# Optimization experiments

Measured on AMD Instinct MI355X. Metric: run time of the kernel, lower is better.

Reference implementation:

```python
import jax, jax.numpy as jnp
import numpy as np

DIM = 2048
N_HEADS = 16
HEAD_DIM = DIM // N_HEADS
HIDDEN = 8192
BSZ = 2
SEQ = 2048
EPS = 1e-6


def setup_inputs() -> dict:
    key = jax.random.key(0)
    ks = jax.random.split(key, 8)
    x = jax.random.normal(ks[0], (BSZ, SEQ, DIM), dtype=jnp.float32)
    # causal additive mask, broadcastable to [B, H, S, S]
    mask = jnp.where(jnp.tril(jnp.ones((SEQ, SEQ), dtype=bool)), 0.0, -1e9)
    mask = mask[None, None, :, :].astype(jnp.float32)
    s = 0.02
    # torch.nn.Linear weights have shape [out_features, in_features]
    wq = jax.random.normal(ks[1], (DIM, DIM), dtype=jnp.float32) * s
    wk = jax.random.normal(ks[2], (DIM, DIM), dtype=jnp.float32) * s
    wv = jax.random.normal(ks[3], (DIM, DIM), dtype=jnp.float32) * s
    wo = jax.random.normal(ks[4], (DIM, DIM), dtype=jnp.float32) * s
    w1 = jax.random.normal(ks[5], (HIDDEN, DIM), dtype=jnp.float32) * s
    w2 = jax.random.normal(ks[6], (DIM, HIDDEN), dtype=jnp.float32) * s
    attn_norm_w = jnp.ones((DIM,), dtype=jnp.float32)
    ffn_norm_w = jnp.ones((DIM,), dtype=jnp.float32)
    return {"x": x, "mask": mask, "wq": wq, "wk": wk, "wv": wv, "wo": wo,
            "w1": w1, "w2": w2, "attn_norm_w": attn_norm_w, "ffn_norm_w": ffn_norm_w}


def rmsnorm(x, w):
    return x * jax.lax.rsqrt(jnp.mean(x * x, axis=-1, keepdims=True) + EPS) * w


def attention(x, mask, wq, wk, wv, wo):
    b, s, _ = x.shape
    q = (x @ wq.T).reshape(b, s, N_HEADS, HEAD_DIM)
    k = (x @ wk.T).reshape(b, s, N_HEADS, HEAD_DIM)
    v = (x @ wv.T).reshape(b, s, N_HEADS, HEAD_DIM)
    scores = jnp.einsum('bqhd,bkhd->bhqk', q, k) / jnp.sqrt(jnp.float32(HEAD_DIM))
    scores = scores + mask
    probs = jax.nn.softmax(scores, axis=-1)
    out = jnp.einsum('bhqk,bkhd->bqhd', probs, v).reshape(b, s, DIM)
    return out @ wo.T


def reference(x, mask, wq, wk, wv, wo, w1, w2, attn_norm_w, ffn_norm_w):
    h = x + attention(rmsnorm(x, attn_norm_w), mask, wq, wk, wv, wo)
    ffn_in = rmsnorm(h, ffn_norm_w)
    ffn = jax.nn.relu(ffn_in @ w1.T) @ w2.T
    return h + ffn
```

## Files before the change

### kernel.cpp

```cpp
#include <hip/hip_runtime.h>
#include <cstdint>
#include <cstddef>

#define DIM 2048
#define NHEADS 16
#define HD 128
#define HIDDEN 8192
#define BSZ 2
#define SEQ 2048
#define MTOT (BSZ*SEQ)

typedef __bf16 bf16_t;
typedef __bf16 bf16x8 __attribute__((ext_vector_type(8)));
typedef __bf16 bf16x4 __attribute__((ext_vector_type(4)));
typedef float  f32x4  __attribute__((ext_vector_type(4)));

__device__ __forceinline__ void gload16(const void* g, void* lds) {
  __builtin_amdgcn_global_load_lds(
      (const __attribute__((address_space(1))) uint32_t*)g,
      (__attribute__((address_space(3))) uint32_t*)lds, 16, 0, 0);
}

#define BAR() do { __builtin_amdgcn_sched_barrier(0); \
  asm volatile("s_barrier" ::: "memory"); \
  __builtin_amdgcn_sched_barrier(0); } while (0)
#define VMW(N) asm volatile("s_waitcnt vmcnt(" #N ")" ::: "memory")

__global__ void cvt_k(const float* __restrict__ src, bf16_t* __restrict__ dst, int n4) {
  int i = blockIdx.x * blockDim.x + threadIdx.x;
  int stride = gridDim.x * blockDim.x;
  for (; i < n4; i += stride) {
    float4 v = ((const float4*)src)[i];
    bf16x4 o = {(__bf16)v.x, (__bf16)v.y, (__bf16)v.z, (__bf16)v.w};
    ((bf16x4*)dst)[i] = o;
  }
}

__global__ __launch_bounds__(256)
void rmsnorm_k(const float* __restrict__ x, const float* __restrict__ wt,
               bf16_t* __restrict__ out) {
  const int row = blockIdx.x;
  const float* xr = x + (size_t)row * DIM;
  const int tid = threadIdx.x;
  float4 a = ((const float4*)xr)[tid];
  float4 b = ((const float4*)xr)[tid + 256];
  float ss = a.x*a.x + a.y*a.y + a.z*a.z + a.w*a.w
           + b.x*b.x + b.y*b.y + b.z*b.z + b.w*b.w;
  #pragma unroll
  for (int d = 32; d >= 1; d >>= 1) ss += __shfl_xor(ss, d, 64);
  __shared__ float red[4];
  if ((tid & 63) == 0) red[tid >> 6] = ss;
  __syncthreads();
  float tot = red[0] + red[1] + red[2] + red[3];
  float rs = rsqrtf(tot * (1.0f / DIM) + 1e-6f);
  float4 wa = ((const float4*)wt)[tid];
  float4 wb = ((const float4*)wt)[tid + 256];
  bf16x4 oa = {(__bf16)(a.x*rs*wa.x), (__bf16)(a.y*rs*wa.y),
               (__bf16)(a.z*rs*wa.z), (__bf16)(a.w*rs*wa.w)};
  bf16x4 ob = {(__bf16)(b.x*rs*wb.x), (__bf16)(b.y*rs*wb.y),
               (__bf16)(b.z*rs*wb.z), (__bf16)(b.w*rs*wb.w)};
  *(bf16x4*)(out + (size_t)row*DIM + tid*4)        = oa;
  *(bf16x4*)(out + (size_t)row*DIM + 1024 + tid*4) = ob;
}

template<int MH, int NH>
__device__ __forceinline__ void mm16(f32x4 (&acc)[8][4],
                                     const bf16x8 (&aF)[4][2],
                                     const bf16x8 (&bF)[2][2]) {
  __builtin_amdgcn_s_setprio(1);
  #pragma unroll
  for (int mt = 0; mt < 4; ++mt)
    #pragma unroll
    for (int nt = 0; nt < 2; ++nt)
      #pragma unroll
      for (int kk = 0; kk < 2; ++kk)
        acc[MH*4+mt][NH*2+nt] = __builtin_amdgcn_mfma_f32_16x16x32_bf16(
            aF[mt][kk], bF[nt][kk], acc[MH*4+mt][NH*2+nt], 0, 0, 0);
  __builtin_amdgcn_s_setprio(0);
}

__device__ __forceinline__ void rdA4(bf16x8 (&aF)[4][2], const bf16_t* rbase,
                                     int wr, int l16, int g) {
  #pragma unroll
  for (int mt = 0; mt < 4; ++mt)
    #pragma unroll
    for (int kk = 0; kk < 2; ++kk)
      aF[mt][kk] = *(const bf16x8*)((const char*)rbase +
          (wr*64 + mt*16 + l16)*128 + ((((kk<<2) ^ g) ^ (l16 & 7)) << 4));
}
__device__ __forceinline__ void rdB2(bf16x8 (&bF)[2][2], const bf16_t* rbase,
                                     int wc, int l16, int g) {
  #pragma unroll
  for (int nt = 0; nt < 2; ++nt)
    #pragma unroll
    for (int kk = 0; kk < 2; ++kk)
      bF[nt][kk] = *(const bf16x8*)((const char*)rbase +
          (wc*32 + nt*16 + l16)*128 + ((((kk<<2) ^ g) ^ (l16 & 7)) << 4));
}

template<typename OUT_T, bool RELU, bool HAS_RES, bool VT_OUT>
__global__ __launch_bounds__(512, 2)
void gemm8p(const bf16_t* __restrict__ A, const bf16_t* __restrict__ B,
            OUT_T* __restrict__ C, const float* __restrict__ res,
            int M, int N, int K) {
  __shared__ bf16_t sA[2][2][128*64];
  __shared__ bf16_t sB[2][2][128*64];
  const int tid  = threadIdx.x;
  const int lane = tid & 63;
  const int wid  = tid >> 6;
  const int l16  = lane & 15;
  const int g    = lane >> 4;
  const int wr   = wid >> 2;
  const int wc   = wid & 3;

  const int nwg = gridDim.x, bid = blockIdx.x;
  const int qq = nwg >> 3, rr = nwg & 7;
  const int xcd = bid & 7, loc = bid >> 3;
  const int wg = (xcd < rr ? xcd*(qq+1) : rr*(qq+1) + (xcd-rr)*qq) + loc;
  const int nbn = N >> 8;
  const int bm = (wg / nbn) << 8;
  const int bn = (wg % nbn) << 8;

  const int lr  = tid >> 3;
  const int cq8 = (((tid & 7) ^ (lr & 7)) << 3);

  const size_t aR = (size_t)(bm + lr) * K + cq8;
  const size_t bR = (size_t)(bn + ((lr >> 5) << 6) + (lr & 31)) * K + cq8;
  const size_t rowK128 = (size_t)128 * K, rowK64 = (size_t)64 * K, rowK32 = (size_t)32 * K;

  auto stA = [&](int buf, int mh, int kt) {
    const size_t ko = aR + (size_t)kt * 64 + (size_t)mh * rowK64;
    gload16(A + ko,            &sA[buf][mh][wid*512]);
    gload16(A + ko + rowK128,  &sA[buf][mh][4096 + wid*512]);
  };
  auto stB = [&](int buf, int nh, int kt) {
    const size_t ko = bR + (size_t)kt * 64 + (size_t)nh * rowK32;
    gload16(B + ko,              &sB[buf][nh][wid*512]);
    gload16(B + ko + 2*rowK64,   &sB[buf][nh][4096 + wid*512]);
  };

  f32x4 acc[8][4] = {};
  bf16x8 aF[4][2], bLo[2][2], bHi[2][2];

  stA(0, 0, 0); stB(0, 0, 0); stB(0, 1, 0); stA(0, 1, 0);
  stA(1, 0, 1); stB(1, 0, 1); stB(1, 1, 1);
  VMW(6);
  BAR();

  const int ni = K >> 7;
  for (int j = 0; j < ni; ++j) {
    const int t1 = 2*j + 1, t2 = 2*j + 2, t3 = 2*j + 3;
    const bool more = (j + 1 < ni);
    rdA4(aF, &sA[0][0][0], wr, l16, g);
    rdB2(bLo, &sB[0][0][0], wc, l16, g);
    stA(1, 1, t1);
    BAR();
    mm16<0,0>(acc, aF, bLo);
    BAR();
    rdB2(bHi, &sB[0][1][0], wc, l16, g);
    if (more) stA(0, 0, t2);
    BAR();
    mm16<0,1>(acc, aF, bHi);
    BAR();
    rdA4(aF, &sA[0][1][0], wr, l16, g);
    if (more) stB(0, 0, t2);
    BAR();
    mm16<1,1>(acc, aF, bHi);
    BAR();
    if (more) { stB(0, 1, t2); VMW(6); } else { VMW(0); }
    BAR();
    mm16<1,0>(acc, aF, bLo);
    BAR();
    rdA4(aF, &sA[1][0][0], wr, l16, g);
    rdB2(bLo, &sB[1][0][0], wc, l16, g);
    if (more) stA(0, 1, t2);
    BAR();
    mm16<0,0>(acc, aF, bLo);
    BAR();
    rdB2(bHi, &sB[1][1][0], wc, l16, g);
    if (more) stA(1, 0, t3);
    BAR();
    mm16<0,1>(acc, aF, bHi);
    BAR();
    rdA4(aF, &sA[1][1][0], wr, l16, g);
    if (more) stB(1, 0, t3);
    BAR();
    mm16<1,1>(acc, aF, bHi);
    BAR();
    if (more) { stB(1, 1, t3); VMW(6); }
    BAR();
    mm16<1,0>(acc, aF, bLo);
    BAR();
  }

  if (VT_OUT) {
    #pragma unroll
    for (int am = 0; am < 8; ++am) {
      const int row = bm + wr*128 + am*16 + g*4;
      #pragma unroll
      for (int an = 0; an < 4; ++an) {
        const int col = bn + wc*64 + an*16 + l16;
        f32x4 a4 = acc[am][an];
        bf16x4 v4 = {(__bf16)a4[0], (__bf16)a4[1], (__bf16)a4[2], (__bf16)a4[3]};
        *(bf16x4*)((bf16_t*)C +
            (((size_t)(row >> 11) * NHEADS + (col >> 7)) * HD + (col & 127)) * SEQ
            + (row & 2047)) = v4;
      }
    }
  } else {
    #pragma unroll
    for (int am = 0; am < 8; ++am) {
      #pragma unroll
      for (int r = 0; r < 4; ++r) {
        const int row = bm + wr*128 + am*16 + g*4 + r;
        #pragma unroll
        for (int an = 0; an < 4; ++an) {
          const int col = bn + wc*64 + an*16 + l16;
          float v = acc[am][an][r];
          if (HAS_RES) v += res[(size_t)row * N + col];
          if (RELU)    v = fmaxf(v, 0.0f);
          C[(size_t)row * N + col] = (OUT_T)v;
        }
      }
    }
  }
}

template<int MH, int NH>
__device__ __forceinline__ void mm8(f32x4 (&acc)[4][4],
                                    const bf16x8 (&aF)[2][2],
                                    const bf16x8 (&bF)[2][2]) {
  __builtin_amdgcn_s_setprio(1);
  #pragma unroll
  for (int mt = 0; mt < 2; ++mt)
    #pragma unroll
    for (int nt = 0; nt < 2; ++nt)
      #pragma unroll
      for (int kk = 0; kk < 2; ++kk)
        acc[MH*2+mt][NH*2+nt] = __builtin_amdgcn_mfma_f32_16x16x32_bf16(
            aF[mt][kk], bF[nt][kk], acc[MH*2+mt][NH*2+nt], 0, 0, 0);
  __builtin_amdgcn_s_setprio(0);
}

__device__ __forceinline__ void rd2(bf16x8 (&f)[2][2], const bf16_t* rbase,
                                    int wrow, int l16, int g) {
  #pragma unroll
  for (int t = 0; t < 2; ++t)
    #pragma unroll
    for (int kk = 0; kk < 2; ++kk)
      f[t][kk] = *(const bf16x8*)((const char*)rbase +
          (wrow + t*16 + l16)*128 + ((((kk<<2) ^ g) ^ (l16 & 7)) << 4));
}

template<typename OUT_T, bool RELU, bool HAS_RES, bool VT_OUT>
__global__ __launch_bounds__(512, 2)
void gemm8p_n128(const bf16_t* __restrict__ A, const bf16_t* __restrict__ B,
                 OUT_T* __restrict__ C, const float* __restrict__ res,
                 int M, int N, int K) {
  __shared__ bf16_t sA[2][2][128*64];
  __shared__ bf16_t sB[2][2][64*64];
  const int tid  = threadIdx.x;
  const int lane = tid & 63;
  const int wid  = tid >> 6;
  const int l16  = lane & 15;
  const int g    = lane >> 4;
  const int wr   = wid >> 1;
  const int wc   = wid & 1;

  const int nwg = gridDim.x, bid = blockIdx.x;
  const int qq = nwg >> 3, rr = nwg & 7;
  const int xcd = bid & 7, loc = bid >> 3;
  const int wg = (xcd < rr ? xcd*(qq+1) : rr*(qq+1) + (xcd-rr)*qq) + loc;
  const int nbn = N >> 7;
  const int bm = (wg / nbn) << 8;
  const int bn = (wg % nbn) << 7;

  const int lr  = tid >> 3;
  const int cq8 = (((tid & 7) ^ (lr & 7)) << 3);
  const size_t aR = (size_t)(bm + ((lr >> 5) << 6) + (lr & 31)) * K + cq8;
  const size_t bR = (size_t)(bn + ((lr >> 5) << 6) + (lr & 31)) * K + cq8;
  const size_t rowK128 = (size_t)128 * K, rowK32 = (size_t)32 * K;

  auto stA = [&](int buf, int mh, int kt) {
    const size_t ko = aR + (size_t)kt * 64 + (size_t)mh * rowK32;
    gload16(A + ko,            &sA[buf][mh][wid*512]);
    gload16(A + ko + rowK128,  &sA[buf][mh][4096 + wid*512]);
  };
  auto stB = [&](int buf, int nh, int kt) {
    gload16(B + bR + (size_t)kt * 64 + (size_t)nh * rowK32, &sB[buf][nh][wid*512]);
  };

  f32x4 acc[4][4] = {};
  bf16x8 aF[2][2], bLo[2][2], bHi[2][2];

  stA(0, 0, 0); stB(0, 0, 0); stB(0, 1, 0); stA(0, 1, 0);
  stA(1, 0, 1); stB(1, 0, 1); stB(1, 1, 1);
  VMW(4);
  BAR();

  const int ar = wr*32;
  const int br = wc*32;
  const int ni = K >> 7;
  for (int j = 0; j < ni; ++j) {
    const int t1 = 2*j + 1, t2 = 2*j + 2, t3 = 2*j + 3;
    const bool more = (j + 1 < ni);
    rd2(aF,  &sA[0][0][0], ar, l16, g);
    rd2(bLo, &sB[0][0][0], br, l16, g);
    stA(1, 1, t1);
    BAR();
    mm8<0,0>(acc, aF, bLo);
    BAR();
    rd2(bHi, &sB[0][1][0], br, l16, g);
    if (more) stA(0, 0, t2);
    BAR();
    mm8<0,1>(acc, aF, bHi);
    BAR();
    rd2(aF, &sA[0][1][0], ar, l16, g);
    if (more) stB(0, 0, t2);
    BAR();
    mm8<1,1>(acc, aF, bHi);
    BAR();
    if (more) { stB(0, 1, t2); VMW(4); } else { VMW(0); }
    BAR();
    mm8<1,0>(acc, aF, bLo);
    BAR();
    rd2(aF,  &sA[1][0][0], ar, l16, g);
    rd2(bLo, &sB[1][0][0], br, l16, g);
    if (more) stA(0, 1, t2);
    BAR();
    mm8<0,0>(acc, aF, bLo);
    BAR();
    rd2(bHi, &sB[1][1][0], br, l16, g);
    if (more) stA(1, 0, t3);
    BAR();
    mm8<0,1>(acc, aF, bHi);
    BAR();
    rd2(aF, &sA[1][1][0], ar, l16, g);
    if (more) stB(1, 0, t3);
    BAR();
    mm8<1,1>(acc, aF, bHi);
    BAR();
    if (more) { stB(1, 1, t3); VMW(4); }
    BAR();
    mm8<1,0>(acc, aF, bLo);
    BAR();
  }

  if (VT_OUT) {
    #pragma unroll
    for (int am = 0; am < 4; ++am) {
      const int row = bm + wr*64 + am*16 + g*4;
      #pragma unroll
      for (int an = 0; an < 4; ++an) {
        const int col = bn + wc*64 + an*16 + l16;
        f32x4 a4 = acc[am][an];
        bf16x4 v4 = {(__bf16)a4[0], (__bf16)a4[1], (__bf16)a4[2], (__bf16)a4[3]};
        *(bf16x4*)((bf16_t*)C +
            (((size_t)(row >> 11) * NHEADS + (col >> 7)) * HD + (col & 127)) * SEQ
            + (row & 2047)) = v4;
      }
    }
  } else {
    #pragma unroll
    for (int am = 0; am < 4; ++am) {
      #pragma unroll
      for (int r = 0; r < 4; ++r) {
        const int row = bm + wr*64 + am*16 + g*4 + r;
        #pragma unroll
        for (int an = 0; an < 4; ++an) {
          const int col = bn + wc*64 + an*16 + l16;
          float v = acc[am][an][r];
          if (HAS_RES) v += res[(size_t)row * N + col];
          if (RELU)    v = fmaxf(v, 0.0f);
          C[(size_t)row * N + col] = (OUT_T)v;
        }
      }
    }
  }
}

__global__ __launch_bounds__(256, 2)
void attn_k(const bf16_t* __restrict__ Q, const bf16_t* __restrict__ Kk,
            const bf16_t* __restrict__ VT, bf16_t* __restrict__ O) {
  __shared__ bf16_t sK[2][64 * 128];
  __shared__ bf16_t sVT[2][128 * 64];
  __shared__ bf16_t sP[4][32 * 64];
  const int tid = threadIdx.x, lane = tid & 63, w = tid >> 6;
  const int l16 = lane & 15, g = lane >> 4;
  const int b = blockIdx.z, h = blockIdx.y;
  const int qt = b ? (SEQ/128 - 1 - blockIdx.x) : blockIdx.x;
  const int ch = h * HD;
  const size_t gb = (size_t)b * SEQ * DIM;
  const int qbase = qt*128 + w*32;
  const bf16_t* VTh = VT + ((size_t)b * NHEADS + h) * ((size_t)HD * SEQ);

  bf16x8 qf[2][4];
  #pragma unroll
  for (int mt = 0; mt < 2; ++mt)
    #pragma unroll
    for (int kb = 0; kb < 4; ++kb)
      qf[mt][kb] = *(const bf16x8*)(Q + gb + (size_t)(qbase + mt*16 + l16)*DIM + ch + kb*32 + g*8);

  f32x4 o[2][8] = {};
  float m_r[2][4], l_r[2][4];
  #pragma unroll
  for (int mt = 0; mt < 2; ++mt)
    #pragma unroll
    for (int r = 0; r < 4; ++r) { m_r[mt][r] = -1e9f; l_r[mt][r] = 0.0f; }

  const float rs = 0.08838834764831845f;
  const int nsteps = (qt*128 + 128) >> 6;

  auto stageK = [&](int buf, int kv0) {
    #pragma unroll
    for (int i = 0; i < 4; ++i) {
      const int c = i*256 + tid;
      const int kv = c >> 4, pos = c & 15;
      const int qsrc = pos ^ (kv & 7);
      gload16(Kk + gb + (size_t)(kv0 + kv)*DIM + ch + (qsrc << 3),
              (char*)sK[buf] + (size_t)(i*256 + w*64)*16);
    }
  };
  auto stageVT = [&](int buf, int kv0) {
    #pragma unroll
    for (int i = 0; i < 4; ++i) {
      const int c = i*256 + tid;
      const int d = c >> 3, p = c & 7;
      const int q = p ^ (d & 7);
      gload16(VTh + (size_t)d * SEQ + kv0 + (q << 3),
              (char*)sVT[buf] + (size_t)(i*256 + w*64)*16);
    }
  };

  stageK(0, 0);  stageVT(0, 0);
  if (nsteps > 1) { stageK(1, 64); stageVT(1, 64); }
  __syncthreads();

  int cur = 0;
  for (int t = 0; t < nsteps; ++t) {
    const int kv0 = t << 6;
    const bool active = (kv0 < qbase + 32);
    if (active) {
      f32x4 s[2][4] = {};
      const char* kb_ = (const char*)sK[cur];
      #pragma unroll
      for (int nt = 0; nt < 4; ++nt) {
        const int row = nt*16 + l16;
        #pragma unroll
        for (int kbi = 0; kbi < 4; ++kbi) {
          const int pos = (kbi*4 + g) ^ (l16 & 7);
          bf16x8 kf = *(const bf16x8*)(kb_ + row*256 + (pos << 4));
          #pragma unroll
          for (int mt = 0; mt < 2; ++mt)
            s[mt][nt] = __builtin_amdgcn_mfma_f32_16x16x32_bf16(qf[mt][kbi], kf, s[mt][nt], 0, 0, 0);
        }
      }

      const bool needmask = (kv0 + 63 > qbase);
      char* pb = (char*)sP[w];
      #pragma unroll
      for (int mt = 0; mt < 2; ++mt) {
        #pragma unroll
        for (int r = 0; r < 4; ++r) {
          const int qpos = qbase + mt*16 + g*4 + r;
          float sv[4];
          #pragma unroll
          for (int nt = 0; nt < 4; ++nt) {
            sv[nt] = s[mt][nt][r] * rs;
            if (needmask && (kv0 + nt*16 + l16 > qpos)) sv[nt] = -1e9f;
          }
          float mx = fmaxf(fmaxf(sv[0], sv[1]), fmaxf(sv[2], sv[3]));
          #pragma unroll
          for (int d = 8; d >= 1; d >>= 1) mx = fmaxf(mx, __shfl_xor(mx, d, 16));
          const float mo = m_r[mt][r];
          if (mx > mo) {
            const float sc = __expf(mo - mx);
            l_r[mt][r] *= sc;
            #pragma unroll
            for (int dt = 0; dt < 8; ++dt) o[mt][dt][r] *= sc;
            m_r[mt][r] = mx;
          }
          const float mn = m_r[mt][r];
          float p[4], rsum = 0.0f;
          #pragma unroll
          for (int nt = 0; nt < 4; ++nt) { p[nt] = __expf(sv[nt] - mn); rsum += p[nt]; }
          #pragma unroll
          for (int d = 8; d >= 1; d >>= 1) rsum += __shfl_xor(rsum, d, 16);
          l_r[mt][r] += rsum;
          const int prow = mt*16 + g*4 + r;
          #pragma unroll
          for (int nt = 0; nt < 4; ++nt)
            *(bf16_t*)(pb + ((prow*128 + nt*32 + l16*2) ^ (g << 5))) = (bf16_t)p[nt];
        }
      }

      bf16x8 pa[2][2];
      #pragma unroll
      for (int mt = 0; mt < 2; ++mt) {
        const int row2 = mt*16 + l16;
        #pragma unroll
        for (int ks = 0; ks < 2; ++ks)
          pa[mt][ks] = *(const bf16x8*)((const char*)sP[w] +
                    ((row2*128 + ks*64 + g*16) ^ (((l16 >> 2) & 3) << 5)));
      }

      const char* vb_ = (const char*)sVT[cur];
      #pragma unroll
      for (int dt = 0; dt < 8; ++dt) {
        const int d = dt*16 + l16;
        #pragma unroll
        for (int ks = 0; ks < 2; ++ks) {
          const int pos = (ks*4 + g) ^ (d & 7);
          bf16x8 vf = *(const bf16x8*)(vb_ + d*128 + (pos << 4));
          #pragma unroll
          for (int mt = 0; mt < 2; ++mt)
            o[mt][dt] = __builtin_amdgcn_mfma_f32_16x16x32_bf16(pa[mt][ks], vf, o[mt][dt], 0, 0, 0);
        }
      }
    }
    __syncthreads();
    if (t + 2 < nsteps) {
      stageK(cur, (t + 2) << 6);
      stageVT(cur, (t + 2) << 6);
    }
    cur ^= 1;
  }

  #pragma unroll
  for (int mt = 0; mt < 2; ++mt) {
    #pragma unroll
    for (int r = 0; r < 4; ++r) {
      const float inv = 1.0f / l_r[mt][r];
      const int row = qbase + mt*16 + g*4 + r;
      #pragma unroll
      for (int dt = 0; dt < 8; ++dt)
        O[gb + (size_t)row*DIM + ch + dt*16 + l16] = (bf16_t)(o[mt][dt][r] * inv);
    }
  }
}

extern "C" void kernel_launch(void* const* d_in, const int* in_sizes, int n_in,
                              void* d_out, int out_size, void* d_ws, size_t ws_size,
                              hipStream_t stream) {
  const float* x   = (const float*)d_in[0];
  const float* wq  = (const float*)d_in[2];
  const float* wk  = (const float*)d_in[3];
  const float* wv  = (const float*)d_in[4];
  const float* wo  = (const float*)d_in[5];
  const float* w1  = (const float*)d_in[6];
  const float* w2  = (const float*)d_in[7];
  const float* anw = (const float*)d_in[8];
  const float* fnw = (const float*)d_in[9];
  float* out = (float*)d_out;

  char* p = (char*)d_ws;
  bf16_t* wqb = (bf16_t*)p; p += (size_t)DIM*DIM*2;
  bf16_t* wkb = (bf16_t*)p; p += (size_t)DIM*DIM*2;
  bf16_t* wvb = (bf16_t*)p; p += (size_t)DIM*DIM*2;
  bf16_t* wob = (bf16_t*)p; p += (size_t)DIM*DIM*2;
  bf16_t* w1b = (bf16_t*)p; p += (size_t)DIM*HIDDEN*2;
  bf16_t* w2b = (bf16_t*)p; p += (size_t)DIM*HIDDEN*2;
  bf16_t* xn  = (bf16_t*)p; p += (size_t)MTOT*DIM*2;
  float*  hb  = (float*)p;  p += (size_t)MTOT*DIM*4;
  bf16_t* big = (bf16_t*)p; p += (size_t)MTOT*HIDDEN*2;
  bf16_t* qb = big;
  bf16_t* kb = big + (size_t)MTOT*DIM;
  bf16_t* vT = big + 2*(size_t)MTOT*DIM;
  bf16_t* ab = big + 3*(size_t)MTOT*DIM;
  bf16_t* f1 = big;

  auto cvt = [&](const float* s, bf16_t* d, size_t n) {
    int n4 = (int)(n / 4);
    int blocks = (n4 + 255) / 256; if (blocks > 4096) blocks = 4096;
    cvt_k<<<blocks, 256, 0, stream>>>(s, d, n4);
  };
  cvt(wq, wqb, (size_t)DIM*DIM);
  cvt(wk, wkb, (size_t)DIM*DIM);
  cvt(wv, wvb, (size_t)DIM*DIM);
  cvt(wo, wob, (size_t)DIM*DIM);
  cvt(w1, w1b, (size_t)DIM*HIDDEN);
  cvt(w2, w2b, (size_t)DIM*HIDDEN);

  rmsnorm_k<<<MTOT, 256, 0, stream>>>(x, anw, xn);

  gemm8p_n128<bf16_t, false, false, false><<<256, 512, 0, stream>>>(xn, wqb, qb, nullptr, MTOT, DIM, DIM);
  gemm8p_n128<bf16_t, false, false, false><<<256, 512, 0, stream>>>(xn, wkb, kb, nullptr, MTOT, DIM, DIM);
  gemm8p_n128<bf16_t, false, false, true ><<<256, 512, 0, stream>>>(xn, wvb, vT, nullptr, MTOT, DIM, DIM);

  attn_k<<<dim3(SEQ/128, NHEADS, BSZ), 256, 0, stream>>>(qb, kb, vT, ab);

  gemm8p_n128<float, false, true, false><<<256, 512, 0, stream>>>(ab, wob, hb, x, MTOT, DIM, DIM);

  rmsnorm_k<<<MTOT, 256, 0, stream>>>(hb, fnw, xn);

  gemm8p<bf16_t, true, false, false><<<512, 512, 0, stream>>>(xn, w1b, f1, nullptr, MTOT, HIDDEN, DIM);

  gemm8p_n128<float, false, true, false><<<256, 512, 0, stream>>>(f1, w2b, out, hb, MTOT, DIM, HIDDEN);
}
```

Baseline: 657.1 us.

## Fuse QKV projection, batch weight casts, split-K FFN down-proj, exp2 softmax

Merges the six weight-conversion launches into one kernel and the three Q/K/V projections into a single GEMM over the concatenated weight, with an epilogue that routes each tile to q, k, or the transposed v buffer. The FFN down-projection switches to a split-K-by-2 run of the 256x256 GEMM that writes two fp32 partials, followed by a reduction kernel that adds the residual. In attention, the softmax scale and log2(e) are folded into Q once so the loop can use exp2f, and MFMA sections are bracketed with setprio. This cuts launch overhead and adds wave parallelism, at the cost of extra fp32 partial traffic, an extra reduction pass, and a bf16 rounding of the scaled Q.

Result: no change. 650.8 us (-1.0%).

```diff
diff --git a/kernel.cpp b/kernel.cpp
--- a/kernel.cpp
+++ b/kernel.cpp
@@ -26,11 +26,25 @@
   __builtin_amdgcn_sched_barrier(0); } while (0)
 #define VMW(N) asm volatile("s_waitcnt vmcnt(" #N ")" ::: "memory")
 
-__global__ void cvt_k(const float* __restrict__ src, bf16_t* __restrict__ dst, int n4) {
+__global__ void cvt_all_k(const float* __restrict__ wq, const float* __restrict__ wk,
+                          const float* __restrict__ wv, const float* __restrict__ wo,
+                          const float* __restrict__ w1, const float* __restrict__ w2,
+                          bf16_t* __restrict__ dst) {
+  const int S1 = (DIM*DIM) >> 2;
+  const int S2 = (DIM*HIDDEN) >> 2;
+  const int total = 4*S1 + 2*S2;
   int i = blockIdx.x * blockDim.x + threadIdx.x;
-  int stride = gridDim.x * blockDim.x;
-  for (; i < n4; i += stride) {
-    float4 v = ((const float4*)src)[i];
+  const int stride = gridDim.x * blockDim.x;
+  for (; i < total; i += stride) {
+    const float* src; int off;
+    if (i < 4*S1) {
+      const int r = i >> 20; off = i & (S1 - 1);
+      src = (r == 0) ? wq : (r == 1) ? wk : (r == 2) ? wv : wo;
+    } else {
+      const int j = i - 4*S1;
+      if (j < S2) { src = w1; off = j; } else { src = w2; off = j - S2; }
+    }
+    float4 v = ((const float4*)src)[off];
     bf16x4 o = {(__bf16)v.x, (__bf16)v.y, (__bf16)v.z, (__bf16)v.w};
     ((bf16x4*)dst)[i] = o;
   }
@@ -63,6 +77,19 @@
   *(bf16x4*)(out + (size_t)row*DIM + 1024 + tid*4) = ob;
 }
 
+__global__ void reduce2_k(const float* __restrict__ hb, const float* __restrict__ p1,
+                          float* __restrict__ out, int n4) {
+  int i = blockIdx.x * blockDim.x + threadIdx.x;
+  const int stride = gridDim.x * blockDim.x;
+  for (; i < n4; i += stride) {
+    float4 a = ((const float4*)out)[i];
+    float4 h = ((const float4*)hb)[i];
+    float4 b = ((const float4*)p1)[i];
+    float4 o = {h.x + a.x + b.x, h.y + a.y + b.y, h.z + a.z + b.z, h.w + a.w + b.w};
+    ((float4*)out)[i] = o;
+  }
+}
+
 template<int MH, int NH>
 __device__ __forceinline__ void mm16(f32x4 (&acc)[8][4],
                                      const bf16x8 (&aF)[4][2],
@@ -98,11 +125,11 @@
           (wc*32 + nt*16 + l16)*128 + ((((kk<<2) ^ g) ^ (l16 & 7)) << 4));
 }
 
-template<typename OUT_T, bool RELU, bool HAS_RES, bool VT_OUT>
+template<typename OUT_T, bool RELU, bool HAS_RES, int SPLIT>
 __global__ __launch_bounds__(512, 2)
 void gemm8p(const bf16_t* __restrict__ A, const bf16_t* __restrict__ B,
             OUT_T* __restrict__ C, const float* __restrict__ res,
-            int M, int N, int K) {
+            int M, int N, int K, int Klen) {
   __shared__ bf16_t sA[2][2][128*64];
   __shared__ bf16_t sB[2][2][128*64];
   const int tid  = threadIdx.x;
@@ -117,9 +144,18 @@
   const int qq = nwg >> 3, rr = nwg & 7;
   const int xcd = bid & 7, loc = bid >> 3;
   const int wg = (xcd < rr ? xcd*(qq+1) : rr*(qq+1) + (xcd-rr)*qq) + loc;
+
+  int tile = wg;
+  if (SPLIT > 1) {
+    const int slice = wg % SPLIT;
+    tile = wg / SPLIT;
+    A += (size_t)slice * Klen;
+    B += (size_t)slice * Klen;
+    if (slice) C = (OUT_T*)res;
+  }
   const int nbn = N >> 8;
-  const int bm = (wg / nbn) << 8;
-  const int bn = (wg % nbn) << 8;
+  const int bm = (tile / nbn) << 8;
+  const int bn = (tile % nbn) << 8;
 
   const int lr  = tid >> 3;
   const int cq8 = (((tid & 7) ^ (lr & 7)) << 3);
@@ -147,7 +183,7 @@
   VMW(6);
   BAR();
 
-  const int ni = K >> 7;
+  const int ni = Klen >> 7;
   for (int j = 0; j < ni; ++j) {
     const int t1 = 2*j + 1, t2 = 2*j + 2, t3 = 2*j + 3;
     const bool more = (j + 1 < ni);
@@ -193,34 +229,18 @@
     BAR();
   }
 
-  if (VT_OUT) {
-    #pragma unroll
-    for (int am = 0; am < 8; ++am) {
-      const int row = bm + wr*128 + am*16 + g*4;
+  #pragma unroll
+  for (int am = 0; am < 8; ++am) {
+    #pragma unroll
+    for (int r = 0; r < 4; ++r) {
+      const int row = bm + wr*128 + am*16 + g*4 + r;
       #pragma unroll
       for (int an = 0; an < 4; ++an) {
         const int col = bn + wc*64 + an*16 + l16;
-        f32x4 a4 = acc[am][an];
-        bf16x4 v4 = {(__bf16)a4[0], (__bf16)a4[1], (__bf16)a4[2], (__bf16)a4[3]};
-        *(bf16x4*)((bf16_t*)C +
-            (((size_t)(row >> 11) * NHEADS + (col >> 7)) * HD + (col & 127)) * SEQ
-            + (row & 2047)) = v4;
-      }
-    }
-  } else {
-    #pragma unroll
-    for (int am = 0; am < 8; ++am) {
-      #pragma unroll
-      for (int r = 0; r < 4; ++r) {
-        const int row = bm + wr*128 + am*16 + g*4 + r;
-        #pragma unroll
-        for (int an = 0; an < 4; ++an) {
-          const int col = bn + wc*64 + an*16 + l16;
-          float v = acc[am][an][r];
-          if (HAS_RES) v += res[(size_t)row * N + col];
-          if (RELU)    v = fmaxf(v, 0.0f);
-          C[(size_t)row * N + col] = (OUT_T)v;
-        }
+        float v = acc[am][an][r];
+        if (HAS_RES) v += res[(size_t)row * N + col];
+        if (RELU)    v = fmaxf(v, 0.0f);
+        C[(size_t)row * N + col] = (OUT_T)v;
       }
     }
   }
@@ -252,7 +272,7 @@
           (wrow + t*16 + l16)*128 + ((((kk<<2) ^ g) ^ (l16 & 7)) << 4));
 }
 
-template<typename OUT_T, bool RELU, bool HAS_RES, bool VT_OUT>
+template<typename OUT_T, bool RELU, bool HAS_RES, int OMODE>
 __global__ __launch_bounds__(512, 2)
 void gemm8p_n128(const bf16_t* __restrict__ A, const bf16_t* __restrict__ B,
                  OUT_T* __restrict__ C, const float* __restrict__ res,
@@ -346,18 +366,37 @@
     BAR();
   }
 
-  if (VT_OUT) {
-    #pragma unroll
-    for (int am = 0; am < 4; ++am) {
-      const int row = bm + wr*64 + am*16 + g*4;
-      #pragma unroll
-      for (int an = 0; an < 4; ++an) {
-        const int col = bn + wc*64 + an*16 + l16;
-        f32x4 a4 = acc[am][an];
-        bf16x4 v4 = {(__bf16)a4[0], (__bf16)a4[1], (__bf16)a4[2], (__bf16)a4[3]};
-        *(bf16x4*)((bf16_t*)C +
-            (((size_t)(row >> 11) * NHEADS + (col >> 7)) * HD + (col & 127)) * SEQ
-            + (row & 2047)) = v4;
+  if (OMODE == 2) {
+    const int t = bn >> 11;
+    const int clb = bn & 2047;
+    if (t < 2) {
+      bf16_t* base = (bf16_t*)C + (size_t)t * MTOT * DIM;
+      #pragma unroll
+      for (int am = 0; am < 4; ++am) {
+        #pragma unroll
+        for (int r = 0; r < 4; ++r) {
+          const int row = bm + wr*64 + am*16 + g*4 + r;
+          #pragma unroll
+          for (int an = 0; an < 4; ++an) {
+            const int cl = clb + wc*64 + an*16 + l16;
+            base[(size_t)row * DIM + cl] = (bf16_t)acc[am][an][r];
+          }
+        }
+      }
+    } else {
+      bf16_t* vbase = (bf16_t*)C + (size_t)2 * MTOT * DIM;
+      #pragma unroll
+      for (int am = 0; am < 4; ++am) {
+        const int row = bm + wr*64 + am*16 + g*4;
+        #pragma unroll
+        for (int an = 0; an < 4; ++an) {
+          const int cl = clb + wc*64 + an*16 + l16;
+          f32x4 a4 = acc[am][an];
+          bf16x4 v4 = {(__bf16)a4[0], (__bf16)a4[1], (__bf16)a4[2], (__bf16)a4[3]};
+          *(bf16x4*)(vbase +
+              (((size_t)(row >> 11) * NHEADS + (cl >> 7)) * HD + (cl & 127)) * SEQ
+              + (row & 2047)) = v4;
+        }
       }
     }
   } else {
@@ -401,6 +440,15 @@
     for (int kb = 0; kb < 4; ++kb)
       qf[mt][kb] = *(const bf16x8*)(Q + gb + (size_t)(qbase + mt*16 + l16)*DIM + ch + kb*32 + g*8);
 
+  const float qs = 0.08838834764831845f * 1.44269504088896f;
+  #pragma unroll
+  for (int mt = 0; mt < 2; ++mt)
+    #pragma unroll
+    for (int kb = 0; kb < 4; ++kb)
+      #pragma unroll
+      for (int e = 0; e < 8; ++e)
+        qf[mt][kb][e] = (__bf16)((float)qf[mt][kb][e] * qs);
+
   f32x4 o[2][8] = {};
   float m_r[2][4], l_r[2][4];
   #pragma unroll
@@ -408,7 +456,6 @@
     #pragma unroll
     for (int r = 0; r < 4; ++r) { m_r[mt][r] = -1e9f; l_r[mt][r] = 0.0f; }
 
-  const float rs = 0.08838834764831845f;
   const int nsteps = (qt*128 + 128) >> 6;
 
   auto stageK = [&](int buf, int kv0) {
@@ -443,6 +490,7 @@
     if (active) {
       f32x4 s[2][4] = {};
       const char* kb_ = (const char*)sK[cur];
+      __builtin_amdgcn_s_setprio(1);
       #pragma unroll
       for (int nt = 0; nt < 4; ++nt) {
         const int row = nt*16 + l16;
@@ -455,6 +503,7 @@
             s[mt][nt] = __builtin_amdgcn_mfma_f32_16x16x32_bf16(qf[mt][kbi], kf, s[mt][nt], 0, 0, 0);
         }
       }
+      __builtin_amdgcn_s_setprio(0);
 
       const bool needmask = (kv0 + 63 > qbase);
       char* pb = (char*)sP[w];
@@ -466,7 +515,7 @@
           float sv[4];
           #pragma unroll
           for (int nt = 0; nt < 4; ++nt) {
-            sv[nt] = s[mt][nt][r] * rs;
+            sv[nt] = s[mt][nt][r];
             if (needmask && (kv0 + nt*16 + l16 > qpos)) sv[nt] = -1e9f;
           }
           float mx = fmaxf(fmaxf(sv[0], sv[1]), fmaxf(sv[2], sv[3]));
@@ -474,7 +523,7 @@
           for (int d = 8; d >= 1; d >>= 1) mx = fmaxf(mx, __shfl_xor(mx, d, 16));
           const float mo = m_r[mt][r];
           if (mx > mo) {
-            const float sc = __expf(mo - mx);
+            const float sc = exp2f(mo - mx);
             l_r[mt][r] *= sc;
             #pragma unroll
             for (int dt = 0; dt < 8; ++dt) o[mt][dt][r] *= sc;
@@ -483,7 +532,7 @@
           const float mn = m_r[mt][r];
           float p[4], rsum = 0.0f;
           #pragma unroll
-          for (int nt = 0; nt < 4; ++nt) { p[nt] = __expf(sv[nt] - mn); rsum += p[nt]; }
+          for (int nt = 0; nt < 4; ++nt) { p[nt] = exp2f(sv[nt] - mn); rsum += p[nt]; }
           #pragma unroll
           for (int d = 8; d >= 1; d >>= 1) rsum += __shfl_xor(rsum, d, 16);
           l_r[mt][r] += rsum;
@@ -505,6 +554,7 @@
       }
 
       const char* vb_ = (const char*)sVT[cur];
+      __builtin_amdgcn_s_setprio(1);
       #pragma unroll
       for (int dt = 0; dt < 8; ++dt) {
         const int d = dt*16 + l16;
@@ -517,6 +567,7 @@
             o[mt][dt] = __builtin_amdgcn_mfma_f32_16x16x32_bf16(pa[mt][ks], vf, o[mt][dt], 0, 0, 0);
         }
       }
+      __builtin_amdgcn_s_setprio(0);
     }
     __syncthreads();
     if (t + 2 < nsteps) {
@@ -554,46 +605,45 @@
   float* out = (float*)d_out;
 
   char* p = (char*)d_ws;
-  bf16_t* wqb = (bf16_t*)p; p += (size_t)DIM*DIM*2;
-  bf16_t* wkb = (bf16_t*)p; p += (size_t)DIM*DIM*2;
-  bf16_t* wvb = (bf16_t*)p; p += (size_t)DIM*DIM*2;
-  bf16_t* wob = (bf16_t*)p; p += (size_t)DIM*DIM*2;
+  bf16_t* wqb = (bf16_t*)p; p += (size_t)DIM*DIM*2*4;
   bf16_t* w1b = (bf16_t*)p; p += (size_t)DIM*HIDDEN*2;
   bf16_t* w2b = (bf16_t*)p; p += (size_t)DIM*HIDDEN*2;
   bf16_t* xn  = (bf16_t*)p; p += (size_t)MTOT*DIM*2;
   float*  hb  = (float*)p;  p += (size_t)MTOT*DIM*4;
   bf16_t* big = (bf16_t*)p; p += (size_t)MTOT*HIDDEN*2;
+  float*  part1 = (float*)p; p += (size_t)MTOT*DIM*4;
+  const bool splitk_ok = ((size_t)(p - (char*)d_ws) <= ws_size);
+
+  bf16_t* wob = wqb + 3*(size_t)DIM*DIM;
   bf16_t* qb = big;
   bf16_t* kb = big + (size_t)MTOT*DIM;
   bf16_t* vT = big + 2*(size_t)MTOT*DIM;
   bf16_t* ab = big + 3*(size_t)MTOT*DIM;
   bf16_t* f1 = big;
 
-  auto cvt = [&](const float* s, bf16_t* d, size_t n) {
-    int n4 = (int)(n / 4);
-    int blocks = (n4 + 255) / 256; if (blocks > 4096) blocks = 4096;
-    cvt_k<<<blocks, 256, 0, stream>>>(s, d, n4);
-  };
-  cvt(wq, wqb, (size_t)DIM*DIM);
-  cvt(wk, wkb, (size_t)DIM*DIM);
-  cvt(wv, wvb, (size_t)DIM*DIM);
-  cvt(wo, wob, (size_t)DIM*DIM);
-  cvt(w1, w1b, (size_t)DIM*HIDDEN);
-  cvt(w2, w2b, (size_t)DIM*HIDDEN);
+  cvt_all_k<<<4096, 256, 0, stream>>>(wq, wk, wv, wo, w1, w2, wqb);
 
   rmsnorm_k<<<MTOT, 256, 0, stream>>>(x, anw, xn);
 
-  gemm8p_n128<bf16_t, false, false, false><<<256, 512, 0, stream>>>(xn, wqb, qb, nullptr, MTOT, DIM, DIM);
-  gemm8p_n128<bf16_t, false, false, false><<<256, 512, 0, stream>>>(xn, wkb, kb, nullptr, MTOT, DIM, DIM);
-  gemm8p_n128<bf16_t, false, false, true ><<<256, 512, 0, stream>>>(xn, wvb, vT, nullptr, MTOT, DIM, DIM);
+  gemm8p_n128<bf16_t, false, false, 2><<<768, 512, 0, stream>>>(
+      xn, wqb, qb, nullptr, MTOT, 3*DIM, DIM);
 
   attn_k<<<dim3(SEQ/128, NHEADS, BSZ), 256, 0, stream>>>(qb, kb, vT, ab);
 
-  gemm8p_n128<float, false, true, false><<<256, 512, 0, stream>>>(ab, wob, hb, x, MTOT, DIM, DIM);
+  gemm8p_n128<float, false, true, 0><<<256, 512, 0, stream>>>(
+      ab, wob, hb, x, MTOT, DIM, DIM);
 
   rmsnorm_k<<<MTOT, 256, 0, stream>>>(hb, fnw, xn);
 
-  gemm8p<bf16_t, true, false, false><<<512, 512, 0, stream>>>(xn, w1b, f1, nullptr, MTOT, HIDDEN, DIM);
-
-  gemm8p_n128<float, false, true, false><<<256, 512, 0, stream>>>(f1, w2b, out, hb, MTOT, DIM, HIDDEN);
-}
+  gemm8p<bf16_t, true, false, 1><<<512, 512, 0, stream>>>(
+      xn, w1b, f1, nullptr, MTOT, HIDDEN, DIM, DIM);
+
+  if (splitk_ok) {
+    gemm8p<float, false, false, 2><<<256, 512, 0, stream>>>(
+        f1, w2b, out, (const float*)part1, MTOT, DIM, HIDDEN, HIDDEN/2);
+    reduce2_k<<<2048, 256, 0, stream>>>(hb, part1, out, MTOT*DIM/4);
+  } else {
+    gemm8p_n128<float, false, true, 0><<<256, 512, 0, stream>>>(
+        f1, w2b, out, hb, MTOT, DIM, HIDDEN);
+  }
+}
```
